# Kernel tuning notes

Hardware: AMD Instinct MI355X
Metric: run time of the kernel (lower is better)

Reference implementation:

```python
import jax, jax.numpy as jnp
import numpy as np

TAU = 2.0      # LIF membrane time constant (spikingjelly default)
VTH = 1.0      # firing threshold
ALPHA = 4.0    # sigmoid surrogate sharpness
EPS = 1e-5     # BatchNorm eps
NUM_HEADS = 12

@jax.custom_vjp
def heaviside(x):
    return (x >= 0.0).astype(x.dtype)

def _h_fwd(x):
    return heaviside(x), x

def _h_bwd(x, g):
    s = jax.nn.sigmoid(ALPHA * x)
    return (g * ALPHA * s * (1.0 - s),)

heaviside.defvjp(_h_fwd, _h_bwd)

def lif(x):
    """Multi-step LIF over leading T axis. hard reset to 0, decay_input."""
    def step(v, xt):
        v = v + (xt - v) / TAU
        s = heaviside(v - VTH)
        return v * (1.0 - s), s
    _, spikes = jax.lax.scan(step, jnp.zeros_like(x[0]), x)
    return spikes

def bn(x, p, axis):
    """Inference BatchNorm; p = stacked (gamma, beta, mean, var) of shape [4, C]."""
    shape = [1] * x.ndim
    shape[axis] = -1
    g, b, m, v = (p[i].reshape(shape) for i in range(4))
    return (x - m) * (g * jax.lax.rsqrt(v + EPS)) + b

def setup_inputs() -> dict:
    key = jax.random.key(0)
    ks = jax.random.split(key, 16)
    T, B, C, H, W = 4, 16, 768, 16, 16
    Ch = 4 * C
    sC = 1.0 / np.sqrt(C)
    sCh = 1.0 / np.sqrt(Ch)
    def bn_pack(k, c):
        return jax.random.uniform(k, (4, c), jnp.float32, 0.1, 1.0)
    return {
        "x": jax.random.normal(ks[0], (T, B, C, H, W), jnp.float32),
        "w_q": jax.random.normal(ks[1], (C, C), jnp.float32) * sC,
        "bn_q": bn_pack(ks[2], C),
        "w_k": jax.random.normal(ks[3], (C, C), jnp.float32) * sC,
        "bn_k": bn_pack(ks[4], C),
        "w_p": jax.random.normal(ks[5], (C, C), jnp.float32) * sC,
        "b_p": jax.random.normal(ks[6], (C,), jnp.float32) * 0.05,
        "bn_p": bn_pack(ks[7], C),
        "w1": jax.random.normal(ks[8], (Ch, C), jnp.float32) * sC,
        "b1": jax.random.normal(ks[9], (Ch,), jnp.float32) * 0.05,
        "bn1": bn_pack(ks[10], Ch),
        "w2": jax.random.normal(ks[11], (C, Ch), jnp.float32) * sCh,
        "b2": jax.random.normal(ks[12], (C,), jnp.float32) * 0.05,
        "bn2": bn_pack(ks[13], C),
    }

def reference(x, w_q, bn_q, w_k, bn_k, w_p, b_p, bn_p, w1, b1, bn1, w2, b2, bn2):
    T, B, C, H, W = x.shape
    N = H * W
    h = NUM_HEADS
    d = C // h
    xf = x.reshape(T, B, C, N)
    # Token QK-less attention: 1x1 conv == channel GEMM, BN, LIF
    q = lif(bn(jnp.einsum('oc,tbcn->tbon', w_q, xf), bn_q, axis=2))
    k = lif(bn(jnp.einsum('oc,tbcn->tbon', w_k, xf), bn_k, axis=2))
    q = q.reshape(T, B, h, d, N)
    k = k.reshape(T, B, h, d, N)
    attn = lif(jnp.sum(q, axis=3, keepdims=True))       # [T,B,h,1,N]
    a = (attn * k).reshape(T, B, C, N)
    p = jnp.einsum('oc,tbcn->tbon', w_p, a) + b_p[None, None, :, None]
    p = lif(bn(p, bn_p, axis=2)).reshape(T, B, C, H, W)
    x = x + p
    # MLP: 1x1 conv2d == channel GEMM, BN, LIF (x2)
    z = jnp.einsum('oc,tbchw->tbohw', w1, x) + b1[None, None, :, None, None]
    z = lif(bn(z, bn1, axis=2))
    z = jnp.einsum('oc,tbchw->tbohw', w2, z) + b2[None, None, :, None, None]
    z = lif(bn(z, bn2, axis=2))
    return x + z
```

## Files before the change

kernel.cpp:

```cpp
#include <hip/hip_runtime.h>

#define T_ 4
#define B_ 16
#define C_ 768
#define N_ 256
#define CH_ 3072

typedef _Float16 f16x8 __attribute__((ext_vector_type(8)));
typedef _Float16 f16x4 __attribute__((ext_vector_type(4)));
typedef float f32x4 __attribute__((ext_vector_type(4)));


__device__ __forceinline__ int xcd_swizzle_linear()
{
    const int ntot = gridDim.x * gridDim.y * gridDim.z;
    const int l0 = blockIdx.x + gridDim.x * (blockIdx.y + gridDim.y * blockIdx.z);
    return (l0 & 7) * (ntot >> 3) + (l0 >> 3);
}

__device__ __forceinline__ void stage_tile(const _Float16* g, _Float16* l,
                                           int wv, int ln)
{
#pragma unroll
    for (int i = 0; i < 2; ++i) {
        const int c = wv * 128 + i * 64;
        __builtin_amdgcn_global_load_lds(
            (const __attribute__((address_space(1))) void*)(g + (size_t)(c + ln) * 8),
            (__attribute__((address_space(3))) void*)(l + (size_t)c * 8),
            16, 0, 0);
    }
}

__device__ __forceinline__ void stage_tile8(const _Float16* g, _Float16* l,
                                            int wv, int ln)
{
    const int c = wv * 64;
    __builtin_amdgcn_global_load_lds(
        (const __attribute__((address_space(1))) void*)(g + (size_t)(c + ln) * 8),
        (__attribute__((address_space(3))) void*)(l + (size_t)c * 8),
        16, 0, 0);
}

template <int NB, int ORD>
__global__ __launch_bounds__(256) void gemm_mfma(
    const _Float16* __restrict__ A0, const _Float16* __restrict__ A1,
    const _Float16* __restrict__ B0, const _Float16* __restrict__ B1,
    float* __restrict__ Oq, float* __restrict__ Ok, int splitBy, int M,
    const float* __restrict__ bias, float oscale,
    int KTA, int ktA0, int mbA0, int KTB, int nkt, int midN)
{
    const int l = xcd_swizzle_linear();
    const int nb = l & 1;
    const int mid = (l >> 1) % midN;
    const int hi  = (l >> 1) / midN;
    const int by = (ORD == 0) ? mid : hi;
    const int bt = (ORD == 0) ? hi  : mid;
    const int mbA = mbA0 + by;

    __shared__ _Float16 lds[2][(2 + NB) * 4096];

    const int tid = threadIdx.x;
    const int wv = tid >> 6;
    const int ln = tid & 63;
    const int mw = (wv >> 1) * 64;
    const int nw = (wv & 1) * 64;

    f32x4 acc[4][4];
#pragma unroll
    for (int i = 0; i < 4; ++i)
#pragma unroll
        for (int j = 0; j < 4; ++j)
            acc[i][j] = (f32x4){0.f, 0.f, 0.f, 0.f};

    const _Float16* ga0 = A0 + ((size_t)mbA * KTA + ktA0) * 4096;
    const _Float16* ga1 = A1 + ((size_t)mbA * KTA + ktA0) * 4096;
    const _Float16* gb0 = B0 + (((size_t)bt * 2 + nb) * KTB) * 4096;
    const _Float16* gb1 = (NB == 2) ? B1 + (((size_t)bt * 2 + nb) * KTB) * 4096 : nullptr;

    const int ca = (ln >> 4) * 128 + mw + (ln & 15);
    const int cb = (ln >> 4) * 128 + nw + (ln & 15);

    _Float16* Lc = &lds[0][0];
    _Float16* Ln = &lds[1][0];

    stage_tile(ga0, Lc, wv, ln);
    stage_tile(ga1, Lc + 4096, wv, ln);
    stage_tile(gb0, Lc + 2 * 4096, wv, ln);
    if (NB == 2) stage_tile(gb1, Lc + 3 * 4096, wv, ln);

    for (int kt = 0; kt < nkt; ++kt) {
        __syncthreads();
        if (kt + 1 < nkt) {
            stage_tile(ga0 + 4096, Ln, wv, ln);
            stage_tile(ga1 + 4096, Ln + 4096, wv, ln);
            stage_tile(gb0 + 4096, Ln + 2 * 4096, wv, ln);
            if (NB == 2) stage_tile(gb1 + 4096, Ln + 3 * 4096, wv, ln);
        }

        f16x8 a0[4], a1[4];
#pragma unroll
        for (int mt = 0; mt < 4; ++mt) {
            a0[mt] = *(const f16x8*)&Lc[(ca + mt * 16) * 8];
            a1[mt] = *(const f16x8*)&Lc[4096 + (ca + mt * 16) * 8];
        }
#pragma unroll
        for (int nt = 0; nt < 4; ++nt) {
            const f16x8 b0 = *(const f16x8*)&Lc[2 * 4096 + (cb + nt * 16) * 8];
            f16x8 b1;
            if (NB == 2) b1 = *(const f16x8*)&Lc[3 * 4096 + (cb + nt * 16) * 8];
#pragma unroll
            for (int mt = 0; mt < 4; ++mt) {
                acc[mt][nt] = __builtin_amdgcn_mfma_f32_16x16x32_f16(a0[mt], b0, acc[mt][nt], 0, 0, 0);
                acc[mt][nt] = __builtin_amdgcn_mfma_f32_16x16x32_f16(a1[mt], b0, acc[mt][nt], 0, 0, 0);
                if (NB == 2)
                    acc[mt][nt] = __builtin_amdgcn_mfma_f32_16x16x32_f16(a0[mt], b1, acc[mt][nt], 0, 0, 0);
            }
        }
        ga0 += 4096; ga1 += 4096; gb0 += 4096;
        if (NB == 2) gb1 += 4096;
        _Float16* tmp = Lc; Lc = Ln; Ln = tmp;
    }

    float* Obase = (by < splitBy) ? Oq : Ok;
    const int byl = (by < splitBy) ? by : by - splitBy;
    float* Ob = Obase + (size_t)bt * M * 256;
    const int lm = (ln >> 4) * 4;
    const int lnn = ln & 15;
#pragma unroll
    for (int mt = 0; mt < 4; ++mt) {
#pragma unroll
        for (int r = 0; r < 4; ++r) {
            const int m = byl * 128 + mw + mt * 16 + lm + r;
            const float bb = bias ? bias[m] : 0.0f;
#pragma unroll
            for (int nt = 0; nt < 4; ++nt) {
                const int n = nb * 128 + nw + nt * 16 + lnn;
                Ob[(size_t)m * 256 + n] = acc[mt][nt][r] * oscale + bb;
            }
        }
    }
}

__global__ __launch_bounds__(512, 2) void gemm_mlp1(
    const _Float16* __restrict__ A0, const _Float16* __restrict__ A1,
    const _Float16* __restrict__ B0, const _Float16* __restrict__ B1,
    const float* __restrict__ bias, const float* __restrict__ bnp,
    _Float16* __restrict__ outB, float oscale)
{
    const int l = xcd_swizzle_linear();
    const int nb = l & 1;
    const int by = (l >> 1) % 24;
    const int b  = (l >> 1) / 24;

    __shared__ _Float16 lds[2][10 * 4096];

    const int tid = threadIdx.x;
    const int wv = tid >> 6;
    const int ln = tid & 63;
    const int mw = (wv >> 2) * 64;
    const int nw = (wv & 3) * 32;
    const int lm = (ln >> 4) * 4;
    const int lnn = ln & 15;

    const _Float16* gA0 = A0 + ((size_t)by * 24) * 4096;
    const _Float16* gA1 = A1 + ((size_t)by * 24) * 4096;
    const _Float16* gB0t[4];
    const _Float16* gB1t[4];
#pragma unroll
    for (int t = 0; t < 4; ++t) {
        const int bt = t * B_ + b;
        gB0t[t] = B0 + (((size_t)bt * 2 + nb) * 24) * 4096;
        gB1t[t] = B1 + (((size_t)bt * 2 + nb) * 24) * 4096;
    }

    f32x4 acc[4][4][2];
#pragma unroll
    for (int t = 0; t < 4; ++t)
#pragma unroll
        for (int i = 0; i < 4; ++i)
#pragma unroll
            for (int j = 0; j < 2; ++j)
                acc[t][i][j] = (f32x4){0.f, 0.f, 0.f, 0.f};

    const int ca = (ln >> 4) * 128 + mw + lnn;
    const int cb = (ln >> 4) * 128 + nw + lnn;

    _Float16* Lc = &lds[0][0];
    _Float16* Ln = &lds[1][0];

    stage_tile8(gA0, Lc, wv, ln);
    stage_tile8(gA1, Lc + 4096, wv, ln);
#pragma unroll
    for (int t = 0; t < 4; ++t) {
        stage_tile8(gB0t[t], Lc + (2 + 2 * t) * 4096, wv, ln);
        stage_tile8(gB1t[t], Lc + (3 + 2 * t) * 4096, wv, ln);
    }

    for (int kt = 0; kt < 24; ++kt) {
        __syncthreads();
        if (kt < 23) {
            const size_t o = (size_t)(kt + 1) * 4096;
            stage_tile8(gA0 + o, Ln, wv, ln);
            stage_tile8(gA1 + o, Ln + 4096, wv, ln);
#pragma unroll
            for (int t = 0; t < 4; ++t) {
                stage_tile8(gB0t[t] + o, Ln + (2 + 2 * t) * 4096, wv, ln);
                stage_tile8(gB1t[t] + o, Ln + (3 + 2 * t) * 4096, wv, ln);
            }
        }

        f16x8 a0[4], a1[4];
#pragma unroll
        for (int mt = 0; mt < 4; ++mt) {
            a0[mt] = *(const f16x8*)&Lc[(ca + mt * 16) * 8];
            a1[mt] = *(const f16x8*)&Lc[4096 + (ca + mt * 16) * 8];
        }
#pragma unroll
        for (int t = 0; t < 4; ++t) {
#pragma unroll
            for (int nt = 0; nt < 2; ++nt) {
                const f16x8 b0 = *(const f16x8*)&Lc[(2 + 2 * t) * 4096 + (cb + nt * 16) * 8];
                const f16x8 b1 = *(const f16x8*)&Lc[(3 + 2 * t) * 4096 + (cb + nt * 16) * 8];
#pragma unroll
                for (int mt = 0; mt < 4; ++mt) {
                    acc[t][mt][nt] = __builtin_amdgcn_mfma_f32_16x16x32_f16(a0[mt], b0, acc[t][mt][nt], 0, 0, 0);
                    acc[t][mt][nt] = __builtin_amdgcn_mfma_f32_16x16x32_f16(a1[mt], b0, acc[t][mt][nt], 0, 0, 0);
                    acc[t][mt][nt] = __builtin_amdgcn_mfma_f32_16x16x32_f16(a0[mt], b1, acc[t][mt][nt], 0, 0, 0);
                }
            }
        }
        _Float16* tmp = Lc; Lc = Ln; Ln = tmp;
    }

    float Af[16], Bf[16];
#pragma unroll
    for (int mt = 0; mt < 4; ++mt)
#pragma unroll
        for (int r = 0; r < 4; ++r) {
            const int c = by * 128 + mw + mt * 16 + lm + r;
            const float g  = bnp[c];
            const float be = bnp[CH_ + c];
            const float mu = bnp[2 * CH_ + c];
            const float va = bnp[3 * CH_ + c];
            const float sc = g * rsqrtf(va + 1e-5f);
            Af[mt * 4 + r] = oscale * sc;
            Bf[mt * 4 + r] = (bias[c] - mu) * sc + be;
        }

#pragma unroll
    for (int mt = 0; mt < 4; ++mt) {
        const int c0m = by * 128 + mw + mt * 16 + lm;
        const int kt_out = c0m >> 5;
        const int k8 = (c0m & 31) >> 3;
        const int j0 = c0m & 7;
#pragma unroll
        for (int nt = 0; nt < 2; ++nt) {
            const int row = nw + nt * 16 + lnn;
            float vv[4] = {0.f, 0.f, 0.f, 0.f};
#pragma unroll
            for (int t = 0; t < 4; ++t) {
                const int bt = t * B_ + b;
                _Float16* ob = outB + (((size_t)bt * 2 + nb) * 96) * 4096;
                f16x4 hh;
#pragma unroll
                for (int r = 0; r < 4; ++r) {
                    const float u = acc[t][mt][nt][r] * Af[mt * 4 + r] + Bf[mt * 4 + r];
                    float xv = vv[r];
                    xv = xv + (u - xv) * 0.5f;
                    const float sp = (xv >= 1.0f) ? 1.0f : 0.0f;
                    vv[r] = (sp > 0.0f) ? 0.0f : xv;
                    hh[r] = (_Float16)sp;
                }
                *(f16x4*)(ob + ((size_t)kt_out * 512 + k8 * 128 + row) * 8 + j0) = hh;
            }
        }
    }
}

__global__ void splitW(const float* __restrict__ W, int ldW,
                       _Float16* __restrict__ C0, _Float16* __restrict__ C1,
                       int KT, float scale)
{
    const int mb = blockIdx.x, kt = blockIdx.y;
    const int mm = threadIdx.x, k8 = threadIdx.y;
    const float* src = W + (size_t)(mb * 128 + mm) * ldW + kt * 32 + k8 * 8;
    const size_t cb = (((size_t)mb * KT + kt) * 512 + k8 * 128 + mm) * 8;
    f16x8 h0, h1;
#pragma unroll
    for (int j = 0; j < 8; ++j) {
        const float x = src[j] * scale;
        const _Float16 h = (_Float16)x;
        h0[j] = h;
        h1[j] = (_Float16)(x - (float)h);
    }
    *(f16x8*)(C0 + cb) = h0;
    *(f16x8*)(C1 + cb) = h1;
}

__global__ void splitW3(const float* __restrict__ wq, const float* __restrict__ wk,
                        const float* __restrict__ wp,
                        _Float16* __restrict__ WQK0, _Float16* __restrict__ WQK1,
                        _Float16* __restrict__ WP0,  _Float16* __restrict__ WP1,
                        float scale)
{
    const size_t WCC = (size_t)C_ * C_;
    const int z = blockIdx.z;
    const float* W;
    _Float16 *C0, *C1;
    if (z == 0)      { W = wq; C0 = WQK0;       C1 = WQK1; }
    else if (z == 1) { W = wk; C0 = WQK0 + WCC; C1 = WQK1 + WCC; }
    else             { W = wp; C0 = WP0;        C1 = WP1; }
    const int mb = blockIdx.x, kt = blockIdx.y;
    const int mm = threadIdx.x, k8 = threadIdx.y;
    const float* src = W + (size_t)(mb * 128 + mm) * C_ + kt * 32 + k8 * 8;
    const size_t cb = (((size_t)mb * 24 + kt) * 512 + k8 * 128 + mm) * 8;
    f16x8 h0, h1;
#pragma unroll
    for (int j = 0; j < 8; ++j) {
        const float x = src[j] * scale;
        const _Float16 h = (_Float16)x;
        h0[j] = h;
        h1[j] = (_Float16)(x - (float)h);
    }
    *(f16x8*)(C0 + cb) = h0;
    *(f16x8*)(C1 + cb) = h1;
}

__global__ void splitB(const float* __restrict__ X,
                       _Float16* __restrict__ C0, _Float16* __restrict__ C1,
                       int KT, float scale)
{
    const int nb = blockIdx.x, kt = blockIdx.y, bt = blockIdx.z;
    const int nn = threadIdx.x, k8 = threadIdx.y;
    const int K = KT * 32;
    const float* src = X + ((size_t)bt * K + kt * 32 + k8 * 8) * 256 + nb * 128 + nn;
    const size_t cb = ((((size_t)bt * 2 + nb) * KT + kt) * 512 + k8 * 128 + nn) * 8;
    f16x8 h0, h1;
#pragma unroll
    for (int j = 0; j < 8; ++j) {
        const float x = src[(size_t)j * 256] * scale;
        const _Float16 h = (_Float16)x;
        h0[j] = h;
        h1[j] = (_Float16)(x - (float)h);
    }
    *(f16x8*)(C0 + cb) = h0;
    *(f16x8*)(C1 + cb) = h1;
}

__global__ __launch_bounds__(512) void qattn_kernel(
    const float* __restrict__ qpre, const float* __restrict__ bnp,
    float* __restrict__ attn)
{
    const int tx = threadIdx.x, ty = threadIdx.y;
    const int n = blockIdx.x * 64 + tx;
    const int h = blockIdx.y, b = blockIdx.z;
    __shared__ float red[8][64];

    float sc[8], be[8], mu[8];
#pragma unroll
    for (int j = 0; j < 8; ++j) {
        const int c = h * 64 + ty * 8 + j;
        const float g = bnp[c];
        be[j] = bnp[C_ + c];
        mu[j] = bnp[2 * C_ + c];
        sc[j] = g * rsqrtf(bnp[3 * C_ + c] + 1e-5f);
    }
    float v[8];
#pragma unroll
    for (int j = 0; j < 8; ++j) v[j] = 0.f;
    float va = 0.f;

#pragma unroll
    for (int t = 0; t < T_; ++t) {
        const int bt = t * B_ + b;
        const float* p = qpre + ((size_t)bt * C_ + h * 64 + ty * 8) * 256 + n;
        float s = 0.f;
#pragma unroll
        for (int j = 0; j < 8; ++j) {
            const float u = (p[(size_t)j * 256] - mu[j]) * sc[j] + be[j];
            v[j] = v[j] + (u - v[j]) * 0.5f;
            const float sp = (v[j] >= 1.0f) ? 1.0f : 0.0f;
            v[j] = (sp > 0.0f) ? 0.0f : v[j];
            s += sp;
        }
        red[ty][tx] = s;
        __syncthreads();
        if (ty == 0) {
            float tot = red[0][tx];
#pragma unroll
            for (int r = 1; r < 8; ++r) tot += red[r][tx];
            va = va + (tot - va) * 0.5f;
            const float asp = (va >= 1.0f) ? 1.0f : 0.0f;
            va = (asp > 0.0f) ? 0.0f : va;
            attn[((size_t)bt * 12 + h) * 256 + n] = asp;
        }
        __syncthreads();
    }
}

__global__ void bnlifB(const float* __restrict__ pre,
                       const float* __restrict__ attn,
                       const float* __restrict__ bnp,
                       int Cc, int Cs, int c0,
                       _Float16* __restrict__ outB, int KTout, int ktOut0)
{
    const int nb = blockIdx.x, kt = blockIdx.y, b = blockIdx.z;
    const int nn = threadIdx.x, k8 = threadIdx.y;
    const int cl = kt * 32 + k8 * 8;
    const int n = nb * 128 + nn;
    float sc[8], be[8], mu[8];
#pragma unroll
    for (int j = 0; j < 8; ++j) {
        const int c = c0 + cl + j;
        const float g = bnp[c];
        be[j] = bnp[Cs + c];
        mu[j] = bnp[2 * Cs + c];
        sc[j] = g * rsqrtf(bnp[3 * Cs + c] + 1e-5f);
    }
    float v[8];
#pragma unroll
    for (int j = 0; j < 8; ++j) v[j] = 0.f;
    const int h = cl >> 6;
#pragma unroll
    for (int t = 0; t < T_; ++t) {
        const int bt = t * B_ + b;
        const float* p = pre + ((size_t)bt * Cc + cl) * 256 + n;
        const float av = attn ? attn[((size_t)bt * 12 + h) * 256 + n] : 1.f;
        f16x8 s;
#pragma unroll
        for (int j = 0; j < 8; ++j) {
            const float u = (p[(size_t)j * 256] - mu[j]) * sc[j] + be[j];
            v[j] = v[j] + (u - v[j]) * 0.5f;
            const float sp = (v[j] >= 1.0f) ? 1.0f : 0.0f;
            v[j] = (sp > 0.0f) ? 0.0f : v[j];
            s[j] = (_Float16)(sp * av);
        }
        *(f16x8*)(outB + ((((size_t)bt * 2 + nb) * KTout + ktOut0 + kt) * 512 + k8 * 128 + nn) * 8) = s;
    }
}

__global__ void bnlif_y_split(const float* __restrict__ ppre,
                              const float* __restrict__ x,
                              const float* __restrict__ bnp,
                              _Float16* __restrict__ Y0, _Float16* __restrict__ Y1,
                              float xscale)
{
    const int nb = blockIdx.x, kt = blockIdx.y, b = blockIdx.z;
    const int nn = threadIdx.x, k8 = threadIdx.y;
    const int cl = kt * 32 + k8 * 8;
    const int n = nb * 128 + nn;
    float sc[8], be[8], mu[8];
#pragma unroll
    for (int j = 0; j < 8; ++j) {
        const int c = cl + j;
        const float g = bnp[c];
        be[j] = bnp[C_ + c];
        mu[j] = bnp[2 * C_ + c];
        sc[j] = g * rsqrtf(bnp[3 * C_ + c] + 1e-5f);
    }
    float v[8];
#pragma unroll
    for (int j = 0; j < 8; ++j) v[j] = 0.f;
#pragma unroll
    for (int t = 0; t < T_; ++t) {
        const int bt = t * B_ + b;
        const size_t off = ((size_t)bt * C_ + cl) * 256 + n;
        const float* p = ppre + off;
        const float* xx = x + off;
        f16x8 h0, h1;
#pragma unroll
        for (int j = 0; j < 8; ++j) {
            const float u = (p[(size_t)j * 256] - mu[j]) * sc[j] + be[j];
            v[j] = v[j] + (u - v[j]) * 0.5f;
            const float sp = (v[j] >= 1.0f) ? 1.0f : 0.0f;
            v[j] = (sp > 0.0f) ? 0.0f : v[j];
            const float ys = (xx[(size_t)j * 256] + sp) * xscale;
            const _Float16 hh = (_Float16)ys;
            h0[j] = hh;
            h1[j] = (_Float16)(ys - (float)hh);
        }
        const size_t cb = ((((size_t)bt * 2 + nb) * 24 + kt) * 512 + k8 * 128 + nn) * 8;
        *(f16x8*)(Y0 + cb) = h0;
        *(f16x8*)(Y1 + cb) = h1;
    }
}

__global__ void bnlif_out(const float* __restrict__ z2,
                          const _Float16* __restrict__ Y0,
                          const _Float16* __restrict__ Y1,
                          const float* __restrict__ bnp,
                          float* __restrict__ out, float yinv)
{
    const int nb = blockIdx.x, kt = blockIdx.y, b = blockIdx.z;
    const int nn = threadIdx.x, k8 = threadIdx.y;
    const int cl = kt * 32 + k8 * 8;
    const int n = nb * 128 + nn;
    float sc[8], be[8], mu[8];
#pragma unroll
    for (int j = 0; j < 8; ++j) {
        const int c = cl + j;
        const float g = bnp[c];
        be[j] = bnp[C_ + c];
        mu[j] = bnp[2 * C_ + c];
        sc[j] = g * rsqrtf(bnp[3 * C_ + c] + 1e-5f);
    }
    float v[8];
#pragma unroll
    for (int j = 0; j < 8; ++j) v[j] = 0.f;
#pragma unroll
    for (int t = 0; t < T_; ++t) {
        const int bt = t * B_ + b;
        const size_t off = ((size_t)bt * C_ + cl) * 256 + n;
        const float* zp = z2 + off;
        float* op = out + off;
        const size_t ycb = ((((size_t)bt * 2 + nb) * 24 + kt) * 512 + k8 * 128 + nn) * 8;
        const f16x8 y0 = *(const f16x8*)(Y0 + ycb);
        const f16x8 y1 = *(const f16x8*)(Y1 + ycb);
#pragma unroll
        for (int j = 0; j < 8; ++j) {
            const float u = (zp[(size_t)j * 256] - mu[j]) * sc[j] + be[j];
            v[j] = v[j] + (u - v[j]) * 0.5f;
            const float sp = (v[j] >= 1.0f) ? 1.0f : 0.0f;
            v[j] = (sp > 0.0f) ? 0.0f : v[j];
            const float y = ((float)y0[j] + (float)y1[j]) * yinv;
            op[(size_t)j * 256] = y + sp;
        }
    }
}

extern "C" void kernel_launch(void* const* d_in, const int* in_sizes, int n_in,
                              void* d_out, int out_size, void* d_ws, size_t ws_size,
                              hipStream_t stream) {
    const float* x    = (const float*)d_in[0];
    const float* w_q  = (const float*)d_in[1];
    const float* bn_q = (const float*)d_in[2];
    const float* w_k  = (const float*)d_in[3];
    const float* bn_k = (const float*)d_in[4];
    const float* w_p  = (const float*)d_in[5];
    const float* b_p  = (const float*)d_in[6];
    const float* bn_p = (const float*)d_in[7];
    const float* w1   = (const float*)d_in[8];
    const float* b1   = (const float*)d_in[9];
    const float* bn1  = (const float*)d_in[10];
    const float* w2   = (const float*)d_in[11];
    const float* b2   = (const float*)d_in[12];
    const float* bn2  = (const float*)d_in[13];

    const size_t SZ1 = (size_t)T_ * B_ * C_ * N_;
    const size_t SZA = (size_t)T_ * B_ * 12 * N_;
    const size_t WCC = (size_t)C_ * C_;
    const size_t WCH = (size_t)C_ * CH_;

    char* w = (char*)d_ws;
    float*     qbuf  = (float*)w;     w += SZ1 * 4;
    float*     attnb = (float*)w;     w += SZA * 4;
    _Float16*  R1    = (_Float16*)w;  w += SZ1 * 4;
    _Float16*  WQK0  = (_Float16*)w;  w += WCC * 2 * 2;
    _Float16*  WQK1  = (_Float16*)w;  w += WCC * 2 * 2;
    _Float16*  WP0   = (_Float16*)w;  w += WCC * 2;
    _Float16*  WP1   = (_Float16*)w;  w += WCC * 2;
    _Float16*  W10   = (_Float16*)w;  w += WCH * 2;
    _Float16*  W11   = (_Float16*)w;  w += WCH * 2;
    _Float16*  W20   = (_Float16*)w;  w += WCH * 2;
    _Float16*  W21   = (_Float16*)w;  w += WCH * 2;
    _Float16*  s1B   = (_Float16*)w;

    _Float16* XB0 = R1;
    _Float16* XB1 = R1 + SZ1;
    _Float16* aB  = R1;
    _Float16* YB0 = R1;
    _Float16* YB1 = R1 + SZ1;

    float* dob = (float*)d_out;

    const float WS = 4096.f;
    const float XS = 256.f;
    const float OS_G = 1.f / 1048576.f;
    const float OS_S = 1.f / 4096.f;

    const dim3 blk256(256);
    const dim3 blkS(128, 4);

    splitW3<<<dim3(6, 24, 3), blkS, 0, stream>>>(w_q, w_k, w_p, WQK0, WQK1, WP0, WP1, WS);
    splitW<<<dim3(24, 24), blkS, 0, stream>>>(w1, C_,  W10, W11, 24, WS);
    splitW<<<dim3(6, 96),  blkS, 0, stream>>>(w2, CH_, W20, W21, 96, WS);
    splitB<<<dim3(2, 24, 64), blkS, 0, stream>>>(x, XB0, XB1, 24, XS);

    gemm_mfma<2, 0><<<dim3(2, 12, 64), blk256, 0, stream>>>(
        WQK0, WQK1, XB0, XB1, qbuf, dob, 6, C_, nullptr, OS_G, 24, 0, 0, 24, 24, 12);

    qattn_kernel<<<dim3(4, 12, B_), dim3(64, 8), 0, stream>>>(qbuf, bn_q, attnb);
    bnlifB<<<dim3(2, 24, B_), blkS, 0, stream>>>(dob, attnb, bn_k, C_, C_, 0, aB, 24, 0);

    gemm_mfma<1, 0><<<dim3(2, 6, 64), blk256, 0, stream>>>(
        WP0, WP1, aB, nullptr, qbuf, nullptr, 9999, C_, b_p, OS_S, 24, 0, 0, 24, 24, 6);
    bnlif_y_split<<<dim3(2, 24, B_), blkS, 0, stream>>>(qbuf, x, bn_p, YB0, YB1, XS);

    gemm_mlp1<<<dim3(2, 24, B_), dim3(512), 0, stream>>>(
        W10, W11, YB0, YB1, b1, bn1, s1B, OS_G);

    gemm_mfma<1, 1><<<dim3(2, 6, 64), blk256, 0, stream>>>(
        W20, W21, s1B, nullptr, dob, nullptr, 9999, C_, b2, OS_S, 96, 0, 0, 96, 96, 64);

    bnlif_out<<<dim3(2, 24, B_), blkS, 0, stream>>>(dob, YB0, YB1, bn2, dob, 1.f / XS);
}
```

Measured before the change: 657.8 us.

## Split MLP1 k-loop into per-timestep phases with fine-grained vmcnt barriers

Restructures the gemm_mlp1 main loop into four phases per k-step, one per timestep. Each phase issues its slice of next-tile global loads and then waits only for the vmcnt needed for the current slice, instead of one full __syncthreads before all loads. MFMA blocks are wrapped in s_setprio to favour matrix issue, and the last iteration is peeled with decreasing wait counts. The aim is to overlap global-to-LDS staging with MFMA work more finely. Correctness now depends on the hand-chosen vmcnt values matching how stage_tile8 issues its loads.

```diff
diff --git a/kernel.cpp b/kernel.cpp
--- a/kernel.cpp
+++ b/kernel.cpp
@@ -141,6 +141,53 @@
     }
 }
 
+
+#define MLP1_MMA(T)                                                           \
+    {                                                                         \
+        f16x8 bb0[2], bb1[2];                                                 \
+        bb0[0] = *(const f16x8*)&Lc[(2 + 2 * (T)) * 4096 + cb * 8];           \
+        bb0[1] = *(const f16x8*)&Lc[(2 + 2 * (T)) * 4096 + (cb + 16) * 8];    \
+        bb1[0] = *(const f16x8*)&Lc[(3 + 2 * (T)) * 4096 + cb * 8];           \
+        bb1[1] = *(const f16x8*)&Lc[(3 + 2 * (T)) * 4096 + (cb + 16) * 8];    \
+        __builtin_amdgcn_s_setprio(1);                                        \
+        _Pragma("unroll")                                                     \
+        for (int nt = 0; nt < 2; ++nt) {                                      \
+            _Pragma("unroll")                                                 \
+            for (int mt = 0; mt < 4; ++mt) {                                  \
+                acc[T][mt][nt] = __builtin_amdgcn_mfma_f32_16x16x32_f16(a0[mt], bb0[nt], acc[T][mt][nt], 0, 0, 0); \
+                acc[T][mt][nt] = __builtin_amdgcn_mfma_f32_16x16x32_f16(a1[mt], bb0[nt], acc[T][mt][nt], 0, 0, 0); \
+                acc[T][mt][nt] = __builtin_amdgcn_mfma_f32_16x16x32_f16(a0[mt], bb1[nt], acc[T][mt][nt], 0, 0, 0); \
+            }                                                                 \
+        }                                                                     \
+        __builtin_amdgcn_s_setprio(0);                                        \
+    }
+
+#define MLP1_WB(VM)                                                           \
+    asm volatile("s_waitcnt vmcnt(" #VM ")\n\ts_barrier" ::: "memory");
+
+#define MLP1_P0(VM, STG)                                                      \
+    MLP1_WB(VM)                                                               \
+    if (STG) {                                                                \
+        stage_tile8(gA0 + o, Ln, wv, ln);                                     \
+        stage_tile8(gA1 + o, Ln + 4096, wv, ln);                              \
+        stage_tile8(gB0t[0] + o, Ln + 2 * 4096, wv, ln);                      \
+        stage_tile8(gB1t[0] + o, Ln + 3 * 4096, wv, ln);                      \
+    }                                                                         \
+    _Pragma("unroll")                                                         \
+    for (int mt = 0; mt < 4; ++mt) {                                          \
+        a0[mt] = *(const f16x8*)&Lc[(ca + mt * 16) * 8];                      \
+        a1[mt] = *(const f16x8*)&Lc[4096 + (ca + mt * 16) * 8];               \
+    }                                                                         \
+    MLP1_MMA(0)
+
+#define MLP1_PT(T, VM, STG)                                                   \
+    MLP1_WB(VM)                                                               \
+    if (STG) {                                                                \
+        stage_tile8(gB0t[T] + o, Ln + (2 + 2 * (T)) * 4096, wv, ln);          \
+        stage_tile8(gB1t[T] + o, Ln + (3 + 2 * (T)) * 4096, wv, ln);          \
+    }                                                                         \
+    MLP1_MMA(T)
+
 __global__ __launch_bounds__(512, 2) void gemm_mlp1(
     const _Float16* __restrict__ A0, const _Float16* __restrict__ A1,
     const _Float16* __restrict__ B0, const _Float16* __restrict__ B1,
@@ -190,46 +237,31 @@
 
     stage_tile8(gA0, Lc, wv, ln);
     stage_tile8(gA1, Lc + 4096, wv, ln);
-#pragma unroll
-    for (int t = 0; t < 4; ++t) {
+    stage_tile8(gB0t[0], Lc + 2 * 4096, wv, ln);
+    stage_tile8(gB1t[0], Lc + 3 * 4096, wv, ln);
+#pragma unroll
+    for (int t = 1; t < 4; ++t) {
         stage_tile8(gB0t[t], Lc + (2 + 2 * t) * 4096, wv, ln);
         stage_tile8(gB1t[t], Lc + (3 + 2 * t) * 4096, wv, ln);
     }
 
-    for (int kt = 0; kt < 24; ++kt) {
-        __syncthreads();
-        if (kt < 23) {
-            const size_t o = (size_t)(kt + 1) * 4096;
-            stage_tile8(gA0 + o, Ln, wv, ln);
-            stage_tile8(gA1 + o, Ln + 4096, wv, ln);
-#pragma unroll
-            for (int t = 0; t < 4; ++t) {
-                stage_tile8(gB0t[t] + o, Ln + (2 + 2 * t) * 4096, wv, ln);
-                stage_tile8(gB1t[t] + o, Ln + (3 + 2 * t) * 4096, wv, ln);
-            }
-        }
-
-        f16x8 a0[4], a1[4];
-#pragma unroll
-        for (int mt = 0; mt < 4; ++mt) {
-            a0[mt] = *(const f16x8*)&Lc[(ca + mt * 16) * 8];
-            a1[mt] = *(const f16x8*)&Lc[4096 + (ca + mt * 16) * 8];
-        }
-#pragma unroll
-        for (int t = 0; t < 4; ++t) {
-#pragma unroll
-            for (int nt = 0; nt < 2; ++nt) {
-                const f16x8 b0 = *(const f16x8*)&Lc[(2 + 2 * t) * 4096 + (cb + nt * 16) * 8];
-                const f16x8 b1 = *(const f16x8*)&Lc[(3 + 2 * t) * 4096 + (cb + nt * 16) * 8];
-#pragma unroll
-                for (int mt = 0; mt < 4; ++mt) {
-                    acc[t][mt][nt] = __builtin_amdgcn_mfma_f32_16x16x32_f16(a0[mt], b0, acc[t][mt][nt], 0, 0, 0);
-                    acc[t][mt][nt] = __builtin_amdgcn_mfma_f32_16x16x32_f16(a1[mt], b0, acc[t][mt][nt], 0, 0, 0);
-                    acc[t][mt][nt] = __builtin_amdgcn_mfma_f32_16x16x32_f16(a0[mt], b1, acc[t][mt][nt], 0, 0, 0);
-                }
-            }
-        }
+    f16x8 a0[4], a1[4];
+
+#pragma unroll 1
+    for (int kt = 0; kt < 23; ++kt) {
+        const size_t o = (size_t)(kt + 1) * 4096;
+        MLP1_P0(6, 1)
+        MLP1_PT(1, 8, 1)
+        MLP1_PT(2, 8, 1)
+        MLP1_PT(3, 8, 1)
         _Float16* tmp = Lc; Lc = Ln; Ln = tmp;
+    }
+    {
+        const size_t o = 0; (void)o;
+        MLP1_P0(6, 0)
+        MLP1_PT(1, 4, 0)
+        MLP1_PT(2, 2, 0)
+        MLP1_PT(3, 0, 0)
     }
 
     float Af[16], Bf[16];
```

After: 651.3 us. No clear change (-1.0%).

## Batch all four timesteps per GEMM block to reuse weight tiles across T

Applied to the files above, without the earlier changes.

Replaces the per-(t,b) GEMM kernel with a 512-thread kernel where each block handles all four timesteps for one batch index. A weight tile staged in LDS is then reused across four activation tiles, cutting weight traffic and halving the grid's per-tile load count. The cost is fewer blocks (a quarter as many), more LDS per block and more accumulator registers (32 f32x4 per thread), which may lower occupancy and hurt latency hiding.

```diff
diff --git a/kernel.cpp b/kernel.cpp
--- a/kernel.cpp
+++ b/kernel.cpp
@@ -18,19 +18,6 @@
     return (l0 & 7) * (ntot >> 3) + (l0 >> 3);
 }
 
-__device__ __forceinline__ void stage_tile(const _Float16* g, _Float16* l,
-                                           int wv, int ln)
-{
-#pragma unroll
-    for (int i = 0; i < 2; ++i) {
-        const int c = wv * 128 + i * 64;
-        __builtin_amdgcn_global_load_lds(
-            (const __attribute__((address_space(1))) void*)(g + (size_t)(c + ln) * 8),
-            (__attribute__((address_space(3))) void*)(l + (size_t)c * 8),
-            16, 0, 0);
-    }
-}
-
 __device__ __forceinline__ void stage_tile8(const _Float16* g, _Float16* l,
                                             int wv, int ln)
 {
@@ -41,41 +28,46 @@
         16, 0, 0);
 }
 
-template <int NB, int ORD>
-__global__ __launch_bounds__(256) void gemm_mfma(
+template <int NB>
+__global__ __launch_bounds__(512) void gemm_tb(
     const _Float16* __restrict__ A0, const _Float16* __restrict__ A1,
     const _Float16* __restrict__ B0, const _Float16* __restrict__ B1,
     float* __restrict__ Oq, float* __restrict__ Ok, int splitBy, int M,
     const float* __restrict__ bias, float oscale,
-    int KTA, int ktA0, int mbA0, int KTB, int nkt, int midN)
+    int KTA, int KTB, int nkt, int byN)
 {
     const int l = xcd_swizzle_linear();
     const int nb = l & 1;
-    const int mid = (l >> 1) % midN;
-    const int hi  = (l >> 1) / midN;
-    const int by = (ORD == 0) ? mid : hi;
-    const int bt = (ORD == 0) ? hi  : mid;
-    const int mbA = mbA0 + by;
-
-    __shared__ _Float16 lds[2][(2 + NB) * 4096];
+    const int by = (l >> 1) % byN;
+    const int b  = (l >> 1) / byN;
+
+    __shared__ _Float16 lds[2][(2 + 4 * NB) * 4096];
 
     const int tid = threadIdx.x;
     const int wv = tid >> 6;
     const int ln = tid & 63;
-    const int mw = (wv >> 1) * 64;
-    const int nw = (wv & 1) * 64;
-
-    f32x4 acc[4][4];
-#pragma unroll
-    for (int i = 0; i < 4; ++i)
-#pragma unroll
-        for (int j = 0; j < 4; ++j)
-            acc[i][j] = (f32x4){0.f, 0.f, 0.f, 0.f};
-
-    const _Float16* ga0 = A0 + ((size_t)mbA * KTA + ktA0) * 4096;
-    const _Float16* ga1 = A1 + ((size_t)mbA * KTA + ktA0) * 4096;
-    const _Float16* gb0 = B0 + (((size_t)bt * 2 + nb) * KTB) * 4096;
-    const _Float16* gb1 = (NB == 2) ? B1 + (((size_t)bt * 2 + nb) * KTB) * 4096 : nullptr;
+    const int mw = (wv >> 2) * 64;
+    const int nw = (wv & 3) * 32;
+
+    f32x4 acc[4][4][2];
+#pragma unroll
+    for (int t = 0; t < 4; ++t)
+#pragma unroll
+        for (int i = 0; i < 4; ++i)
+#pragma unroll
+            for (int j = 0; j < 2; ++j)
+                acc[t][i][j] = (f32x4){0.f, 0.f, 0.f, 0.f};
+
+    const _Float16* gA0 = A0 + ((size_t)by * KTA) * 4096;
+    const _Float16* gA1 = A1 + ((size_t)by * KTA) * 4096;
+    const _Float16* gB0t[4];
+    const _Float16* gB1t[4];
+#pragma unroll
+    for (int t = 0; t < 4; ++t) {
+        const int bt = t * B_ + b;
+        gB0t[t] = B0 + (((size_t)bt * 2 + nb) * KTB) * 4096;
+        if (NB == 2) gB1t[t] = B1 + (((size_t)bt * 2 + nb) * KTB) * 4096;
+    }
 
     const int ca = (ln >> 4) * 128 + mw + (ln & 15);
     const int cb = (ln >> 4) * 128 + nw + (ln & 15);
@@ -83,18 +75,25 @@
     _Float16* Lc = &lds[0][0];
     _Float16* Ln = &lds[1][0];
 
-    stage_tile(ga0, Lc, wv, ln);
-    stage_tile(ga1, Lc + 4096, wv, ln);
-    stage_tile(gb0, Lc + 2 * 4096, wv, ln);
-    if (NB == 2) stage_tile(gb1, Lc + 3 * 4096, wv, ln);
+    stage_tile8(gA0, Lc, wv, ln);
+    stage_tile8(gA1, Lc + 4096, wv, ln);
+#pragma unroll
+    for (int t = 0; t < 4; ++t) {
+        stage_tile8(gB0t[t], Lc + (NB == 2 ? (2 + 2 * t) : (2 + t)) * 4096, wv, ln);
+        if (NB == 2) stage_tile8(gB1t[t], Lc + (3 + 2 * t) * 4096, wv, ln);
+    }
 
     for (int kt = 0; kt < nkt; ++kt) {
         __syncthreads();
         if (kt + 1 < nkt) {
-            stage_tile(ga0 + 4096, Ln, wv, ln);
-            stage_tile(ga1 + 4096, Ln + 4096, wv, ln);
-            stage_tile(gb0 + 4096, Ln + 2 * 4096, wv, ln);
-            if (NB == 2) stage_tile(gb1 + 4096, Ln + 3 * 4096, wv, ln);
+            const size_t o = (size_t)(kt + 1) * 4096;
+            stage_tile8(gA0 + o, Ln, wv, ln);
+            stage_tile8(gA1 + o, Ln + 4096, wv, ln);
+#pragma unroll
+            for (int t = 0; t < 4; ++t) {
+                stage_tile8(gB0t[t] + o, Ln + (NB == 2 ? (2 + 2 * t) : (2 + t)) * 4096, wv, ln);
+                if (NB == 2) stage_tile8(gB1t[t] + o, Ln + (3 + 2 * t) * 4096, wv, ln);
+            }
         }
 
         f16x8 a0[4], a1[4];
@@ -104,38 +103,43 @@
             a1[mt] = *(const f16x8*)&Lc[4096 + (ca + mt * 16) * 8];
         }
 #pragma unroll
-        for (int nt = 0; nt < 4; ++nt) {
-            const f16x8 b0 = *(const f16x8*)&Lc[2 * 4096 + (cb + nt * 16) * 8];
-            f16x8 b1;
-            if (NB == 2) b1 = *(const f16x8*)&Lc[3 * 4096 + (cb + nt * 16) * 8];
-#pragma unroll
-            for (int mt = 0; mt < 4; ++mt) {
-                acc[mt][nt] = __builtin_amdgcn_mfma_f32_16x16x32_f16(a0[mt], b0, acc[mt][nt], 0, 0, 0);
-                acc[mt][nt] = __builtin_amdgcn_mfma_f32_16x16x32_f16(a1[mt], b0, acc[mt][nt], 0, 0, 0);
-                if (NB == 2)
-                    acc[mt][nt] = __builtin_amdgcn_mfma_f32_16x16x32_f16(a0[mt], b1, acc[mt][nt], 0, 0, 0);
+        for (int t = 0; t < 4; ++t) {
+#pragma unroll
+            for (int nt = 0; nt < 2; ++nt) {
+                const f16x8 b0 = *(const f16x8*)&Lc[(NB == 2 ? (2 + 2 * t) : (2 + t)) * 4096 + (cb + nt * 16) * 8];
+                f16x8 b1;
+                if (NB == 2) b1 = *(const f16x8*)&Lc[(3 + 2 * t) * 4096 + (cb + nt * 16) * 8];
+#pragma unroll
+                for (int mt = 0; mt < 4; ++mt) {
+                    acc[t][mt][nt] = __builtin_amdgcn_mfma_f32_16x16x32_f16(a0[mt], b0, acc[t][mt][nt], 0, 0, 0);
+                    acc[t][mt][nt] = __builtin_amdgcn_mfma_f32_16x16x32_f16(a1[mt], b0, acc[t][mt][nt], 0, 0, 0);
+                    if (NB == 2)
+                        acc[t][mt][nt] = __builtin_amdgcn_mfma_f32_16x16x32_f16(a0[mt], b1, acc[t][mt][nt], 0, 0, 0);
+                }
             }
         }
-        ga0 += 4096; ga1 += 4096; gb0 += 4096;
-        if (NB == 2) gb1 += 4096;
         _Float16* tmp = Lc; Lc = Ln; Ln = tmp;
     }
 
     float* Obase = (by < splitBy) ? Oq : Ok;
     const int byl = (by < splitBy) ? by : by - splitBy;
-    float* Ob = Obase + (size_t)bt * M * 256;
     const int lm = (ln >> 4) * 4;
     const int lnn = ln & 15;
 #pragma unroll
-    for (int mt = 0; mt < 4; ++mt) {
-#pragma unroll
-        for (int r = 0; r < 4; ++r) {
-            const int m = byl * 128 + mw + mt * 16 + lm + r;
-            const float bb = bias ? bias[m] : 0.0f;
-#pragma unroll
-            for (int nt = 0; nt < 4; ++nt) {
-                const int n = nb * 128 + nw + nt * 16 + lnn;
-                Ob[(size_t)m * 256 + n] = acc[mt][nt][r] * oscale + bb;
+    for (int t = 0; t < 4; ++t) {
+        const int bt = t * B_ + b;
+        float* Ob = Obase + (size_t)bt * M * 256;
+#pragma unroll
+        for (int mt = 0; mt < 4; ++mt) {
+#pragma unroll
+            for (int r = 0; r < 4; ++r) {
+                const int m = byl * 128 + mw + mt * 16 + lm + r;
+                const float bb = bias ? bias[m] : 0.0f;
+#pragma unroll
+                for (int nt = 0; nt < 2; ++nt) {
+                    const int n = nb * 128 + nw + nt * 16 + lnn;
+                    Ob[(size_t)m * 256 + n] = acc[t][mt][nt][r] * oscale + bb;
+                }
             }
         }
     }
@@ -578,7 +582,7 @@
     const float OS_G = 1.f / 1048576.f;
     const float OS_S = 1.f / 4096.f;
 
-    const dim3 blk256(256);
+    const dim3 blk512(512);
     const dim3 blkS(128, 4);
 
     splitW3<<<dim3(6, 24, 3), blkS, 0, stream>>>(w_q, w_k, w_p, WQK0, WQK1, WP0, WP1, WS);
@@ -586,21 +590,21 @@
     splitW<<<dim3(6, 96),  blkS, 0, stream>>>(w2, CH_, W20, W21, 96, WS);
     splitB<<<dim3(2, 24, 64), blkS, 0, stream>>>(x, XB0, XB1, 24, XS);
 
-    gemm_mfma<2, 0><<<dim3(2, 12, 64), blk256, 0, stream>>>(
-        WQK0, WQK1, XB0, XB1, qbuf, dob, 6, C_, nullptr, OS_G, 24, 0, 0, 24, 24, 12);
+    gemm_tb<2><<<dim3(2, 12, B_), blk512, 0, stream>>>(
+        WQK0, WQK1, XB0, XB1, qbuf, dob, 6, C_, nullptr, OS_G, 24, 24, 24, 12);
 
     qattn_kernel<<<dim3(4, 12, B_), dim3(64, 8), 0, stream>>>(qbuf, bn_q, attnb);
     bnlifB<<<dim3(2, 24, B_), blkS, 0, stream>>>(dob, attnb, bn_k, C_, C_, 0, aB, 24, 0);
 
-    gemm_mfma<1, 0><<<dim3(2, 6, 64), blk256, 0, stream>>>(
-        WP0, WP1, aB, nullptr, qbuf, nullptr, 9999, C_, b_p, OS_S, 24, 0, 0, 24, 24, 6);
+    gemm_tb<1><<<dim3(2, 6, B_), blk512, 0, stream>>>(
+        WP0, WP1, aB, nullptr, qbuf, nullptr, 9999, C_, b_p, OS_S, 24, 24, 24, 6);
     bnlif_y_split<<<dim3(2, 24, B_), blkS, 0, stream>>>(qbuf, x, bn_p, YB0, YB1, XS);
 
-    gemm_mlp1<<<dim3(2, 24, B_), dim3(512), 0, stream>>>(
+    gemm_mlp1<<<dim3(2, 24, B_), blk512, 0, stream>>>(
         W10, W11, YB0, YB1, b1, bn1, s1B, OS_G);
 
-    gemm_mfma<1, 1><<<dim3(2, 6, 64), blk256, 0, stream>>>(
-        W20, W21, s1B, nullptr, dob, nullptr, 9999, C_, b2, OS_S, 96, 0, 0, 96, 96, 64);
+    gemm_tb<1><<<dim3(2, 6, B_), blk512, 0, stream>>>(
+        W20, W21, s1B, nullptr, dob, nullptr, 9999, C_, b2, OS_S, 96, 96, 96, 6);
 
     bnlif_out<<<dim3(2, 24, B_), blkS, 0, stream>>>(dob, YB0, YB1, bn2, dob, 1.f / XS);
 }
```

Result: slower. 695.1 us (+5.7%).

## Fuse projection and MLP2 GEMMs with BN+LIF epilogues over all time steps

Applied to the files above, without the earlier changes.

Adds a GEMM kernel where each block computes all four time steps for the same batch/channel/token tile. BN, the LIF recurrence over T, the residual add and the f16 hi/lo split then run in registers in the epilogue. This replaces the separate projection GEMM + bnlif_y_split and the MLP2 GEMM + bnlif_out passes, removing the fp32 pre-activation round trips through global memory. The trade-off is fewer blocks (192 instead of 768), larger LDS (six 4096-element tiles, double-buffered) and many accumulator registers, which may reduce occupancy. The Y buffers are moved to the qbuf region so they do not alias the inputs of the fused projection GEMM.

```diff
diff --git a/kernel.cpp b/kernel.cpp
--- a/kernel.cpp
+++ b/kernel.cpp
@@ -136,6 +136,161 @@
             for (int nt = 0; nt < 4; ++nt) {
                 const int n = nb * 128 + nw + nt * 16 + lnn;
                 Ob[(size_t)m * 256 + n] = acc[mt][nt][r] * oscale + bb;
+            }
+        }
+    }
+}
+
+template <int MODE>
+__global__ __launch_bounds__(512) void gemm_tb_lif(
+    const _Float16* __restrict__ A0, const _Float16* __restrict__ A1,
+    const _Float16* __restrict__ B0,
+    const float* __restrict__ bias, const float* __restrict__ bnp,
+    float oscale, int KT, int nkt,
+    const float* __restrict__ x,
+    _Float16* __restrict__ Y0, _Float16* __restrict__ Y1,
+    float* __restrict__ outp,
+    float sc2)
+{
+    const int l = xcd_swizzle_linear();
+    const int nb = l & 1;
+    const int by = (l >> 1) % 6;
+    const int b  = (l >> 1) / 6;
+
+    __shared__ _Float16 lds[2][6 * 4096];
+
+    const int tid = threadIdx.x;
+    const int wv = tid >> 6;
+    const int ln = tid & 63;
+    const int mw = (wv >> 2) * 64;
+    const int nw = (wv & 3) * 32;
+    const int lm = (ln >> 4) * 4;
+    const int lnn = ln & 15;
+
+    const _Float16* gA0 = A0 + ((size_t)by * KT) * 4096;
+    const _Float16* gA1 = A1 + ((size_t)by * KT) * 4096;
+    const _Float16* gB0t[4];
+#pragma unroll
+    for (int t = 0; t < 4; ++t) {
+        const int bt = t * B_ + b;
+        gB0t[t] = B0 + (((size_t)bt * 2 + nb) * KT) * 4096;
+    }
+
+    f32x4 acc[4][4][2];
+#pragma unroll
+    for (int t = 0; t < 4; ++t)
+#pragma unroll
+        for (int i = 0; i < 4; ++i)
+#pragma unroll
+            for (int j = 0; j < 2; ++j)
+                acc[t][i][j] = (f32x4){0.f, 0.f, 0.f, 0.f};
+
+    const int ca = (ln >> 4) * 128 + mw + lnn;
+    const int cb = (ln >> 4) * 128 + nw + lnn;
+
+    _Float16* Lc = &lds[0][0];
+    _Float16* Ln = &lds[1][0];
+
+    stage_tile8(gA0, Lc, wv, ln);
+    stage_tile8(gA1, Lc + 4096, wv, ln);
+#pragma unroll
+    for (int t = 0; t < 4; ++t)
+        stage_tile8(gB0t[t], Lc + (2 + t) * 4096, wv, ln);
+
+    for (int kt = 0; kt < nkt; ++kt) {
+        __syncthreads();
+        if (kt + 1 < nkt) {
+            const size_t o = (size_t)(kt + 1) * 4096;
+            stage_tile8(gA0 + o, Ln, wv, ln);
+            stage_tile8(gA1 + o, Ln + 4096, wv, ln);
+#pragma unroll
+            for (int t = 0; t < 4; ++t)
+                stage_tile8(gB0t[t] + o, Ln + (2 + t) * 4096, wv, ln);
+        }
+
+        f16x8 a0[4], a1[4];
+#pragma unroll
+        for (int mt = 0; mt < 4; ++mt) {
+            a0[mt] = *(const f16x8*)&Lc[(ca + mt * 16) * 8];
+            a1[mt] = *(const f16x8*)&Lc[4096 + (ca + mt * 16) * 8];
+        }
+#pragma unroll
+        for (int t = 0; t < 4; ++t) {
+#pragma unroll
+            for (int nt = 0; nt < 2; ++nt) {
+                const f16x8 b0 = *(const f16x8*)&Lc[(2 + t) * 4096 + (cb + nt * 16) * 8];
+#pragma unroll
+                for (int mt = 0; mt < 4; ++mt) {
+                    acc[t][mt][nt] = __builtin_amdgcn_mfma_f32_16x16x32_f16(a0[mt], b0, acc[t][mt][nt], 0, 0, 0);
+                    acc[t][mt][nt] = __builtin_amdgcn_mfma_f32_16x16x32_f16(a1[mt], b0, acc[t][mt][nt], 0, 0, 0);
+                }
+            }
+        }
+        _Float16* tmp = Lc; Lc = Ln; Ln = tmp;
+    }
+
+    float Af[16], Bf[16];
+#pragma unroll
+    for (int mt = 0; mt < 4; ++mt)
+#pragma unroll
+        for (int r = 0; r < 4; ++r) {
+            const int c = by * 128 + mw + mt * 16 + lm + r;
+            const float g  = bnp[c];
+            const float be = bnp[C_ + c];
+            const float mu = bnp[2 * C_ + c];
+            const float va = bnp[3 * C_ + c];
+            const float sc = g * rsqrtf(va + 1e-5f);
+            Af[mt * 4 + r] = oscale * sc;
+            Bf[mt * 4 + r] = (bias[c] - mu) * sc + be;
+        }
+
+#pragma unroll
+    for (int mt = 0; mt < 4; ++mt) {
+        const int c0m = by * 128 + mw + mt * 16 + lm;
+        const int kt_out = c0m >> 5;
+        const int k8 = (c0m & 31) >> 3;
+        const int j0 = c0m & 7;
+#pragma unroll
+        for (int nt = 0; nt < 2; ++nt) {
+            const int row = nw + nt * 16 + lnn;
+            const int n = nb * 128 + row;
+            float vv[4] = {0.f, 0.f, 0.f, 0.f};
+#pragma unroll
+            for (int t = 0; t < 4; ++t) {
+                const int bt = t * B_ + b;
+                const size_t ycb = (((size_t)bt * 2 + nb) * 24 + kt_out) * 4096
+                                   + ((size_t)k8 * 128 + row) * 8 + j0;
+                if (MODE == 0) {
+                    f16x4 h0, h1;
+#pragma unroll
+                    for (int r = 0; r < 4; ++r) {
+                        const float u = acc[t][mt][nt][r] * Af[mt * 4 + r] + Bf[mt * 4 + r];
+                        float xv = vv[r];
+                        xv = xv + (u - xv) * 0.5f;
+                        const float sp = (xv >= 1.0f) ? 1.0f : 0.0f;
+                        vv[r] = (sp > 0.0f) ? 0.0f : xv;
+                        const float xr = x[((size_t)bt * C_ + c0m + r) * 256 + n];
+                        const float ys = (xr + sp) * sc2;
+                        const _Float16 hh = (_Float16)ys;
+                        h0[r] = hh;
+                        h1[r] = (_Float16)(ys - (float)hh);
+                    }
+                    *(f16x4*)(Y0 + ycb) = h0;
+                    *(f16x4*)(Y1 + ycb) = h1;
+                } else {
+                    const f16x4 y0 = *(const f16x4*)(Y0 + ycb);
+                    const f16x4 y1 = *(const f16x4*)(Y1 + ycb);
+#pragma unroll
+                    for (int r = 0; r < 4; ++r) {
+                        const float u = acc[t][mt][nt][r] * Af[mt * 4 + r] + Bf[mt * 4 + r];
+                        float xv = vv[r];
+                        xv = xv + (u - xv) * 0.5f;
+                        const float sp = (xv >= 1.0f) ? 1.0f : 0.0f;
+                        vv[r] = (sp > 0.0f) ? 0.0f : xv;
+                        const float y = ((float)y0[r] + (float)y1[r]) * sc2;
+                        outp[((size_t)bt * C_ + c0m + r) * 256 + n] = y + sp;
+                    }
+                }
             }
         }
     }
@@ -436,95 +591,6 @@
             s[j] = (_Float16)(sp * av);
         }
         *(f16x8*)(outB + ((((size_t)bt * 2 + nb) * KTout + ktOut0 + kt) * 512 + k8 * 128 + nn) * 8) = s;
-    }
-}
-
-__global__ void bnlif_y_split(const float* __restrict__ ppre,
-                              const float* __restrict__ x,
-                              const float* __restrict__ bnp,
-                              _Float16* __restrict__ Y0, _Float16* __restrict__ Y1,
-                              float xscale)
-{
-    const int nb = blockIdx.x, kt = blockIdx.y, b = blockIdx.z;
-    const int nn = threadIdx.x, k8 = threadIdx.y;
-    const int cl = kt * 32 + k8 * 8;
-    const int n = nb * 128 + nn;
-    float sc[8], be[8], mu[8];
-#pragma unroll
-    for (int j = 0; j < 8; ++j) {
-        const int c = cl + j;
-        const float g = bnp[c];
-        be[j] = bnp[C_ + c];
-        mu[j] = bnp[2 * C_ + c];
-        sc[j] = g * rsqrtf(bnp[3 * C_ + c] + 1e-5f);
-    }
-    float v[8];
-#pragma unroll
-    for (int j = 0; j < 8; ++j) v[j] = 0.f;
-#pragma unroll
-    for (int t = 0; t < T_; ++t) {
-        const int bt = t * B_ + b;
-        const size_t off = ((size_t)bt * C_ + cl) * 256 + n;
-        const float* p = ppre + off;
-        const float* xx = x + off;
-        f16x8 h0, h1;
-#pragma unroll
-        for (int j = 0; j < 8; ++j) {
-            const float u = (p[(size_t)j * 256] - mu[j]) * sc[j] + be[j];
-            v[j] = v[j] + (u - v[j]) * 0.5f;
-            const float sp = (v[j] >= 1.0f) ? 1.0f : 0.0f;
-            v[j] = (sp > 0.0f) ? 0.0f : v[j];
-            const float ys = (xx[(size_t)j * 256] + sp) * xscale;
-            const _Float16 hh = (_Float16)ys;
-            h0[j] = hh;
-            h1[j] = (_Float16)(ys - (float)hh);
-        }
-        const size_t cb = ((((size_t)bt * 2 + nb) * 24 + kt) * 512 + k8 * 128 + nn) * 8;
-        *(f16x8*)(Y0 + cb) = h0;
-        *(f16x8*)(Y1 + cb) = h1;
-    }
-}
-
-__global__ void bnlif_out(const float* __restrict__ z2,
-                          const _Float16* __restrict__ Y0,
-                          const _Float16* __restrict__ Y1,
-                          const float* __restrict__ bnp,
-                          float* __restrict__ out, float yinv)
-{
-    const int nb = blockIdx.x, kt = blockIdx.y, b = blockIdx.z;
-    const int nn = threadIdx.x, k8 = threadIdx.y;
-    const int cl = kt * 32 + k8 * 8;
-    const int n = nb * 128 + nn;
-    float sc[8], be[8], mu[8];
-#pragma unroll
-    for (int j = 0; j < 8; ++j) {
-        const int c = cl + j;
-        const float g = bnp[c];
-        be[j] = bnp[C_ + c];
-        mu[j] = bnp[2 * C_ + c];
-        sc[j] = g * rsqrtf(bnp[3 * C_ + c] + 1e-5f);
-    }
-    float v[8];
-#pragma unroll
-    for (int j = 0; j < 8; ++j) v[j] = 0.f;
-#pragma unroll
-    for (int t = 0; t < T_; ++t) {
-        const int bt = t * B_ + b;
-        const size_t off = ((size_t)bt * C_ + cl) * 256 + n;
-        const float* zp = z2 + off;
-        float* op = out + off;
-        const size_t ycb = ((((size_t)bt * 2 + nb) * 24 + kt) * 512 + k8 * 128 + nn) * 8;
-        const f16x8 y0 = *(const f16x8*)(Y0 + ycb);
-        const f16x8 y1 = *(const f16x8*)(Y1 + ycb);
-#pragma unroll
-        for (int j = 0; j < 8; ++j) {
-            const float u = (zp[(size_t)j * 256] - mu[j]) * sc[j] + be[j];
-            v[j] = v[j] + (u - v[j]) * 0.5f;
-            const float sp = (v[j] >= 1.0f) ? 1.0f : 0.0f;
-            v[j] = (sp > 0.0f) ? 0.0f : v[j];
-            const float y = ((float)y0[j] + (float)y1[j]) * yinv;
-            op[(size_t)j * 256] = y + sp;
-        }
     }
 }
 
@@ -568,8 +634,8 @@
     _Float16* XB0 = R1;
     _Float16* XB1 = R1 + SZ1;
     _Float16* aB  = R1;
-    _Float16* YB0 = R1;
-    _Float16* YB1 = R1 + SZ1;
+    _Float16* YB0 = (_Float16*)qbuf;
+    _Float16* YB1 = YB0 + SZ1;
 
     float* dob = (float*)d_out;
 
@@ -579,6 +645,7 @@
     const float OS_S = 1.f / 4096.f;
 
     const dim3 blk256(256);
+    const dim3 blk512(512);
     const dim3 blkS(128, 4);
 
     splitW3<<<dim3(6, 24, 3), blkS, 0, stream>>>(w_q, w_k, w_p, WQK0, WQK1, WP0, WP1, WS);
@@ -592,15 +659,14 @@
     qattn_kernel<<<dim3(4, 12, B_), dim3(64, 8), 0, stream>>>(qbuf, bn_q, attnb);
     bnlifB<<<dim3(2, 24, B_), blkS, 0, stream>>>(dob, attnb, bn_k, C_, C_, 0, aB, 24, 0);
 
-    gemm_mfma<1, 0><<<dim3(2, 6, 64), blk256, 0, stream>>>(
-        WP0, WP1, aB, nullptr, qbuf, nullptr, 9999, C_, b_p, OS_S, 24, 0, 0, 24, 24, 6);
-    bnlif_y_split<<<dim3(2, 24, B_), blkS, 0, stream>>>(qbuf, x, bn_p, YB0, YB1, XS);
-
-    gemm_mlp1<<<dim3(2, 24, B_), dim3(512), 0, stream>>>(
+    gemm_tb_lif<0><<<dim3(2, 6, B_), blk512, 0, stream>>>(
+        WP0, WP1, aB, b_p, bn_p, OS_S, 24, 24,
+        x, YB0, YB1, nullptr, XS);
+
+    gemm_mlp1<<<dim3(2, 24, B_), blk512, 0, stream>>>(
         W10, W11, YB0, YB1, b1, bn1, s1B, OS_G);
 
-    gemm_mfma<1, 1><<<dim3(2, 6, 64), blk256, 0, stream>>>(
-        W20, W21, s1B, nullptr, dob, nullptr, 9999, C_, b2, OS_S, 96, 0, 0, 96, 96, 64);
-
-    bnlif_out<<<dim3(2, 24, B_), blkS, 0, stream>>>(dob, YB0, YB1, bn2, dob, 1.f / XS);
-}
+    gemm_tb_lif<1><<<dim3(2, 6, B_), blk512, 0, stream>>>(
+        W20, W21, s1B, b2, bn2, OS_S, 96, 96,
+        nullptr, YB0, YB1, dob, 1.f / XS);
+}
```

Result: no change. 665.0 us (+1.1%).
